# Kernel tuning notes

Measured on AMD Instinct MI355X. Metric: run time of the kernel, lower is better.

## Reference

```python
import jax, jax.numpy as jnp
import numpy as np

N = 1_000_000   # num_nodes
H = 256         # hidden_dim
B = 8           # batch size (number of files/graphs)
F = 256         # number of functions


def setup_inputs() -> dict:
    key = jax.random.key(0)
    k1, k2, k3, k4, k5 = jax.random.split(key, 5)
    x = jax.random.normal(k1, (N, H), dtype=jnp.float32)
    batch = jax.random.randint(k2, (N,), 0, B)
    function_ids = jax.random.randint(k3, (N,), 0, F)
    Wf = jax.random.normal(k4, (H, 2 * H), dtype=jnp.float32) * 0.02  # function_pool Linear weight
    bf = jnp.zeros((H,), jnp.float32)
    Wg = jax.random.normal(k5, (H, 2 * H), dtype=jnp.float32) * 0.02  # file_pool Linear weight
    bg = jnp.zeros((H,), jnp.float32)
    return dict(x=x, batch=batch, function_ids=function_ids, Wf=Wf, bf=bf, Wg=Wg, bg=bg)


def reference(x, batch, function_ids, Wf, bf, Wg, bg):
    # Two-level segment reduce: nodes -> (function, batch) segments -> file.
    seg = function_ids * B + batch                     # (N,) flat segment id
    S = F * B
    ssum = jax.ops.segment_sum(x, seg, num_segments=S)                       # (S, H)
    cnt = jax.ops.segment_sum(jnp.ones((x.shape[0], 1), x.dtype), seg, num_segments=S)
    mean = ssum / jnp.maximum(cnt, 1.0)                                      # segment mean
    smax = jax.ops.segment_max(x, seg, num_segments=S)
    smax = jnp.where(cnt > 0, smax, jnp.zeros((), x.dtype))                  # empty segs -> 0
    feat = jnp.concatenate([mean, smax], axis=-1).reshape(F, B, 2 * H)       # (F, B, 2H)
    # function_pool: Linear(2H -> H) + ReLU (dropout = eval-mode identity)
    func = jax.nn.relu(jnp.einsum('fbk,hk->fbh', feat, Wf) + bf)             # (F, B, H)
    # file-level: mean + max over functions
    file_feat = jnp.concatenate([func.mean(axis=0), func.max(axis=0)], axis=-1)  # (B, 2H)
    return jax.nn.relu(file_feat @ Wg.T + bg)                                # (B, H)
```

## Files before the change

### kernel.cpp

```cpp
#include <hip/hip_runtime.h>
#include <math.h>

#define HDIM 256
#define BSZ 8
#define FNUM 256
#define SEGS (FNUM * BSZ)
#define TWOH 512
#define NBLK 512

__global__ __launch_bounds__(256) void hist_k(const int* __restrict__ batch,
                                              const int* __restrict__ fid,
                                              unsigned short* __restrict__ seg16,
                                              int* __restrict__ hist_t,
                                              int N, int chunk) {
    __shared__ int h[SEGS];
    int p = blockIdx.x, t = threadIdx.x;
    for (int s = t; s < SEGS; s += 256) h[s] = 0;
    __syncthreads();
    int beg = p * chunk;
    int end = beg + chunk; if (end > N) end = N;
    if (beg < end) {
        int nv = (end - beg) >> 2;
        const int4* b4 = (const int4*)(batch + beg);
        const int4* f4 = (const int4*)(fid + beg);
        ushort4* s4 = (ushort4*)(seg16 + beg);
        for (int j = t; j < nv; j += 256) {
            int4 bb = b4[j];
            int4 ff = f4[j];
            int s0 = ff.x * BSZ + bb.x;
            int s1 = ff.y * BSZ + bb.y;
            int s2 = ff.z * BSZ + bb.z;
            int s3 = ff.w * BSZ + bb.w;
            s4[j] = make_ushort4((unsigned short)s0, (unsigned short)s1,
                                 (unsigned short)s2, (unsigned short)s3);
            atomicAdd(&h[s0], 1);
            atomicAdd(&h[s1], 1);
            atomicAdd(&h[s2], 1);
            atomicAdd(&h[s3], 1);
        }
        for (int i = beg + (nv << 2) + t; i < end; i += 256) {
            int s = fid[i] * BSZ + batch[i];
            seg16[i] = (unsigned short)s;
            atomicAdd(&h[s], 1);
        }
    }
    __syncthreads();
    for (int s = t; s < SEGS; s += 256)
        hist_t[(size_t)s * NBLK + p] = h[s];
}

__global__ __launch_bounds__(64) void segscan_k(int* __restrict__ hist_t,
                                                int* __restrict__ cnt) {
    int s = blockIdx.x * 64 + threadIdx.x;
    if (s >= SEGS) return;
    int4* row = (int4*)(hist_t + (size_t)s * NBLK);
    int run = 0;
#pragma unroll 4
    for (int j = 0; j < NBLK / 4; ++j) {
        int4 v = row[j];
        int4 o;
        o.x = run; run += v.x;
        o.y = run; run += v.y;
        o.z = run; run += v.z;
        o.w = run; run += v.w;
        row[j] = o;
    }
    cnt[s] = run;
}

__global__ void scan_k(const int* __restrict__ cnt, int* __restrict__ starts) {
    __shared__ int part[256];
    int t = threadIdx.x;
    int local[8];
    int s = 0;
#pragma unroll
    for (int j = 0; j < 8; ++j) { local[j] = cnt[t * 8 + j]; s += local[j]; }
    part[t] = s;
    __syncthreads();
    for (int off = 1; off < 256; off <<= 1) {
        int v = (t >= off) ? part[t - off] : 0;
        __syncthreads();
        part[t] += v;
        __syncthreads();
    }
    int run = (t == 0) ? 0 : part[t - 1];
#pragma unroll
    for (int j = 0; j < 8; ++j) {
        starts[t * 8 + j] = run;
        run += local[j];
    }
}

__global__ __launch_bounds__(256) void scatter_k(const unsigned short* __restrict__ seg16,
                                                 const int* __restrict__ hist_t,
                                                 const int* __restrict__ starts,
                                                 int* __restrict__ sorted,
                                                 int N, int chunk) {
    __shared__ int off[SEGS];
    int p = blockIdx.x, t = threadIdx.x;
    for (int s = t; s < SEGS; s += 256)
        off[s] = starts[s] + hist_t[(size_t)s * NBLK + p];
    __syncthreads();
    int beg = p * chunk;
    int end = beg + chunk; if (end > N) end = N;
    if (beg < end) {
        int nv = (end - beg) >> 2;
        const ushort4* s4 = (const ushort4*)(seg16 + beg);
        for (int j = t; j < nv; j += 256) {
            ushort4 ss = s4[j];
            int i0 = beg + 4 * j;
            sorted[atomicAdd(&off[ss.x], 1)] = i0;
            sorted[atomicAdd(&off[ss.y], 1)] = i0 + 1;
            sorted[atomicAdd(&off[ss.z], 1)] = i0 + 2;
            sorted[atomicAdd(&off[ss.w], 1)] = i0 + 3;
        }
        for (int i = beg + (nv << 2) + t; i < end; i += 256)
            sorted[atomicAdd(&off[seg16[i]], 1)] = i;
    }
}

__global__ __launch_bounds__(256) void segreduce_k(const float4* __restrict__ x4,
                                                   const int* __restrict__ sorted,
                                                   const int* __restrict__ starts,
                                                   const int* __restrict__ cnt,
                                                   float* __restrict__ feat) {
    __shared__ int sidx[256];
    __shared__ float4 rs[256];
    __shared__ float4 rm[256];
    int s = blockIdx.x;
    int start = starts[s];
    int n = cnt[s];
    int t = threadIdx.x;
    int g = t >> 6;
    int l = t & 63;
    float4 as = make_float4(0.f, 0.f, 0.f, 0.f);
    float4 am = make_float4(-INFINITY, -INFINITY, -INFINITY, -INFINITY);

    for (int base = 0; base < n; base += 256) {
        int lim = n - base;
        if (lim > 256) lim = 256;
        if (t < lim) sidx[t] = sorted[start + base + t];
        __syncthreads();
        for (int r = g; r < lim; r += 4) {
            int idx = sidx[r];
            float4 v = x4[(size_t)idx * 64 + l];
            as.x += v.x; as.y += v.y; as.z += v.z; as.w += v.w;
            am.x = fmaxf(am.x, v.x); am.y = fmaxf(am.y, v.y);
            am.z = fmaxf(am.z, v.z); am.w = fmaxf(am.w, v.w);
        }
        __syncthreads();
    }
    rs[t] = as;
    rm[t] = am;
    __syncthreads();
    if (t < 64) {
#pragma unroll
        for (int j = 1; j < 4; ++j) {
            float4 o = rs[t + 64 * j];
            as.x += o.x; as.y += o.y; as.z += o.z; as.w += o.w;
            float4 m = rm[t + 64 * j];
            am.x = fmaxf(am.x, m.x); am.y = fmaxf(am.y, m.y);
            am.z = fmaxf(am.z, m.z); am.w = fmaxf(am.w, m.w);
        }
        float inv = 1.0f / (float)(n > 0 ? n : 1);
        float4 mean = make_float4(as.x * inv, as.y * inv, as.z * inv, as.w * inv);
        if (n == 0) am = make_float4(0.f, 0.f, 0.f, 0.f);
        float4* fm = (float4*)(feat + (size_t)s * TWOH);
        fm[l] = mean;
        fm[64 + l] = am;
    }
}

__global__ __launch_bounds__(256) void funcpool_k(const float* __restrict__ feat,
                                                  const float4* __restrict__ Wf4,
                                                  const float* __restrict__ bfv,
                                                  float* __restrict__ func) {
    __shared__ float fl[BSZ][TWOH];
    int f = blockIdx.x;
    int t = threadIdx.x;
    const float4* src = (const float4*)(feat + (size_t)f * BSZ * TWOH);
    float4* dst = (float4*)&fl[0][0];
    for (int j = t; j < BSZ * TWOH / 4; j += 256) dst[j] = src[j];
    __syncthreads();
    float acc[BSZ];
#pragma unroll
    for (int b = 0; b < BSZ; ++b) acc[b] = 0.f;
    const float4* wrow = Wf4 + (size_t)t * (TWOH / 4);
    for (int k4 = 0; k4 < TWOH / 4; ++k4) {
        float4 w = wrow[k4];
        int k = k4 * 4;
#pragma unroll
        for (int b = 0; b < BSZ; ++b) {
            acc[b] += w.x * fl[b][k] + w.y * fl[b][k + 1] + w.z * fl[b][k + 2] + w.w * fl[b][k + 3];
        }
    }
    float bias = bfv[t];
#pragma unroll
    for (int b = 0; b < BSZ; ++b) {
        float v = acc[b] + bias;
        func[((size_t)f * BSZ + b) * HDIM + t] = v > 0.f ? v : 0.f;
    }
}

__global__ void filereduce_k(const float* __restrict__ func, float* __restrict__ file_feat) {
    int b = blockIdx.x;
    int t = threadIdx.x;
    float s = 0.f, m = -INFINITY;
    for (int f = 0; f < FNUM; ++f) {
        float v = func[((size_t)f * BSZ + b) * HDIM + t];
        s += v;
        m = fmaxf(m, v);
    }
    file_feat[b * TWOH + t] = s * (1.0f / FNUM);
    file_feat[b * TWOH + HDIM + t] = m;
}

__global__ void final_k(const float* __restrict__ file_feat, const float4* __restrict__ Wg4,
                        const float* __restrict__ bg, float* __restrict__ out) {
    __shared__ float fl[TWOH];
    int b = blockIdx.x;
    int t = threadIdx.x;
    for (int j = t; j < TWOH; j += 256) fl[j] = file_feat[b * TWOH + j];
    __syncthreads();
    float acc = 0.f;
    const float4* wr = Wg4 + (size_t)t * (TWOH / 4);
    for (int k4 = 0; k4 < TWOH / 4; ++k4) {
        float4 w = wr[k4];
        int k = k4 * 4;
        acc += w.x * fl[k] + w.y * fl[k + 1] + w.z * fl[k + 2] + w.w * fl[k + 3];
    }
    float v = acc + bg[t];
    out[b * HDIM + t] = v > 0.f ? v : 0.f;
}

extern "C" void kernel_launch(void* const* d_in, const int* in_sizes, int n_in,
                              void* d_out, int out_size, void* d_ws, size_t ws_size,
                              hipStream_t stream) {
    const float* x = (const float*)d_in[0];
    const int* batch = (const int*)d_in[1];
    const int* fid = (const int*)d_in[2];
    const float* Wf = (const float*)d_in[3];
    const float* bfv = (const float*)d_in[4];
    const float* Wg = (const float*)d_in[5];
    const float* bg = (const float*)d_in[6];
    float* out = (float*)d_out;
    int N = in_sizes[1];

    int* sorted = (int*)d_ws;
    int* hist_t = sorted + N;
    int* starts = hist_t + (size_t)SEGS * NBLK;
    int* cnt = starts + SEGS;
    float* feat = (float*)(cnt + SEGS);
    float* func = feat + (size_t)SEGS * TWOH;
    float* file_feat = func + (size_t)SEGS * HDIM;
    unsigned short* seg16 = (unsigned short*)(file_feat + BSZ * TWOH);

    int chunk = ((N + NBLK - 1) / NBLK + 3) & ~3;

    hist_k<<<NBLK, 256, 0, stream>>>(batch, fid, seg16, hist_t, N, chunk);
    segscan_k<<<SEGS / 64, 64, 0, stream>>>(hist_t, cnt);
    scan_k<<<1, 256, 0, stream>>>(cnt, starts);
    scatter_k<<<NBLK, 256, 0, stream>>>(seg16, hist_t, starts, sorted, N, chunk);
    segreduce_k<<<SEGS, 256, 0, stream>>>((const float4*)x, sorted, starts, cnt, feat);
    funcpool_k<<<FNUM, 256, 0, stream>>>(feat, (const float4*)Wf, bfv, func);
    filereduce_k<<<BSZ, 256, 0, stream>>>(func, file_feat);
    final_k<<<BSZ, 256, 0, stream>>>(file_feat, (const float4*)Wg, bg, out);
}
```

Baseline: 293.6 us.

## Parallelize segment scan per wavefront, unroll gather, fuse file reduce with final linear

The per-segment exclusive scan over block histograms now gives each segment a 64-lane wavefront that scans with shuffles, replacing one serial thread walking 512 entries. This is meant to remove a serial, poorly coalesced pass. The segment-reduce gather loop is unrolled by two so two row loads are in flight per iteration, adding latency hiding. The file-level reduce and the final linear layer are fused into one kernel, which drops a launch and the intermediate buffer.

```diff
diff --git a/kernel.cpp b/kernel.cpp
--- a/kernel.cpp
+++ b/kernel.cpp
@@ -49,23 +49,26 @@
         hist_t[(size_t)s * NBLK + p] = h[s];
 }
 
-__global__ __launch_bounds__(64) void segscan_k(int* __restrict__ hist_t,
-                                                int* __restrict__ cnt) {
-    int s = blockIdx.x * 64 + threadIdx.x;
-    if (s >= SEGS) return;
-    int4* row = (int4*)(hist_t + (size_t)s * NBLK);
-    int run = 0;
-#pragma unroll 4
-    for (int j = 0; j < NBLK / 4; ++j) {
-        int4 v = row[j];
-        int4 o;
-        o.x = run; run += v.x;
-        o.y = run; run += v.y;
-        o.z = run; run += v.z;
-        o.w = run; run += v.w;
-        row[j] = o;
-    }
-    cnt[s] = run;
+__global__ __launch_bounds__(256) void segscan_k(int* __restrict__ hist_t,
+                                                 int* __restrict__ cnt) {
+    int wid = (int)((blockIdx.x * 256 + threadIdx.x) >> 6);
+    int lane = threadIdx.x & 63;
+    if (wid >= SEGS) return;
+    int4* row = (int4*)(hist_t + (size_t)wid * NBLK + lane * 8);
+    int4 a = row[0], b = row[1];
+    int lsum = a.x + a.y + a.z + a.w + b.x + b.y + b.z + b.w;
+    int inc = lsum;
+#pragma unroll
+    for (int off = 1; off < 64; off <<= 1) {
+        int v = __shfl_up(inc, off, 64);
+        if (lane >= off) inc += v;
+    }
+    int r = inc - lsum;
+    int4 oa, ob;
+    oa.x = r; r += a.x; oa.y = r; r += a.y; oa.z = r; r += a.z; oa.w = r; r += a.w;
+    ob.x = r; r += b.x; ob.y = r; r += b.y; ob.z = r; r += b.z; ob.w = r; r += b.w;
+    row[0] = oa; row[1] = ob;
+    if (lane == 63) cnt[wid] = inc;
 }
 
 __global__ void scan_k(const int* __restrict__ cnt, int* __restrict__ starts) {
@@ -141,12 +144,25 @@
         if (lim > 256) lim = 256;
         if (t < lim) sidx[t] = sorted[start + base + t];
         __syncthreads();
-        for (int r = g; r < lim; r += 4) {
-            int idx = sidx[r];
-            float4 v = x4[(size_t)idx * 64 + l];
-            as.x += v.x; as.y += v.y; as.z += v.z; as.w += v.w;
-            am.x = fmaxf(am.x, v.x); am.y = fmaxf(am.y, v.y);
-            am.z = fmaxf(am.z, v.z); am.w = fmaxf(am.w, v.w);
+        int r = g;
+        for (; r + 4 < lim; r += 8) {
+            int i0 = sidx[r];
+            int i1 = sidx[r + 4];
+            float4 v0 = x4[(size_t)i0 * 64 + l];
+            float4 v1 = x4[(size_t)i1 * 64 + l];
+            as.x += v0.x; as.y += v0.y; as.z += v0.z; as.w += v0.w;
+            am.x = fmaxf(am.x, v0.x); am.y = fmaxf(am.y, v0.y);
+            am.z = fmaxf(am.z, v0.z); am.w = fmaxf(am.w, v0.w);
+            as.x += v1.x; as.y += v1.y; as.z += v1.z; as.w += v1.w;
+            am.x = fmaxf(am.x, v1.x); am.y = fmaxf(am.y, v1.y);
+            am.z = fmaxf(am.z, v1.z); am.w = fmaxf(am.w, v1.w);
+        }
+        if (r < lim) {
+            int i0 = sidx[r];
+            float4 v0 = x4[(size_t)i0 * 64 + l];
+            as.x += v0.x; as.y += v0.y; as.z += v0.z; as.w += v0.w;
+            am.x = fmaxf(am.x, v0.x); am.y = fmaxf(am.y, v0.y);
+            am.z = fmaxf(am.z, v0.z); am.w = fmaxf(am.w, v0.w);
         }
         __syncthreads();
     }
@@ -202,25 +218,22 @@
     }
 }
 
-__global__ void filereduce_k(const float* __restrict__ func, float* __restrict__ file_feat) {
+__global__ __launch_bounds__(256) void filefinal_k(const float* __restrict__ func,
+                                                   const float4* __restrict__ Wg4,
+                                                   const float* __restrict__ bg,
+                                                   float* __restrict__ out) {
+    __shared__ float fl[TWOH];
     int b = blockIdx.x;
     int t = threadIdx.x;
     float s = 0.f, m = -INFINITY;
+#pragma unroll 4
     for (int f = 0; f < FNUM; ++f) {
         float v = func[((size_t)f * BSZ + b) * HDIM + t];
         s += v;
         m = fmaxf(m, v);
     }
-    file_feat[b * TWOH + t] = s * (1.0f / FNUM);
-    file_feat[b * TWOH + HDIM + t] = m;
-}
-
-__global__ void final_k(const float* __restrict__ file_feat, const float4* __restrict__ Wg4,
-                        const float* __restrict__ bg, float* __restrict__ out) {
-    __shared__ float fl[TWOH];
-    int b = blockIdx.x;
-    int t = threadIdx.x;
-    for (int j = t; j < TWOH; j += 256) fl[j] = file_feat[b * TWOH + j];
+    fl[t] = s * (1.0f / FNUM);
+    fl[HDIM + t] = m;
     __syncthreads();
     float acc = 0.f;
     const float4* wr = Wg4 + (size_t)t * (TWOH / 4);
@@ -252,17 +265,15 @@
     int* cnt = starts + SEGS;
     float* feat = (float*)(cnt + SEGS);
     float* func = feat + (size_t)SEGS * TWOH;
-    float* file_feat = func + (size_t)SEGS * HDIM;
-    unsigned short* seg16 = (unsigned short*)(file_feat + BSZ * TWOH);
+    unsigned short* seg16 = (unsigned short*)(func + (size_t)SEGS * HDIM);
 
     int chunk = ((N + NBLK - 1) / NBLK + 3) & ~3;
 
     hist_k<<<NBLK, 256, 0, stream>>>(batch, fid, seg16, hist_t, N, chunk);
-    segscan_k<<<SEGS / 64, 64, 0, stream>>>(hist_t, cnt);
+    segscan_k<<<SEGS / 4, 256, 0, stream>>>(hist_t, cnt);
     scan_k<<<1, 256, 0, stream>>>(cnt, starts);
     scatter_k<<<NBLK, 256, 0, stream>>>(seg16, hist_t, starts, sorted, N, chunk);
     segreduce_k<<<SEGS, 256, 0, stream>>>((const float4*)x, sorted, starts, cnt, feat);
     funcpool_k<<<FNUM, 256, 0, stream>>>(feat, (const float4*)Wf, bfv, func);
-    filereduce_k<<<BSZ, 256, 0, stream>>>(func, file_feat);
-    final_k<<<BSZ, 256, 0, stream>>>(file_feat, (const float4*)Wg, bg, out);
-}
+    filefinal_k<<<BSZ, 256, 0, stream>>>(func, (const float4*)Wg, bg, out);
+}
```

New measurement: 291.8 us. Within noise of the previous version (-0.6%).
